# Performance work log

Measured on AMD Instinct MI355X. Metric: run time of the kernel, lower is better.

## Reference

```python
import jax, jax.numpy as jnp
import numpy as np

HEAD = 4
HW_DIM = 256  # in_dim // 2


def _gconv1x1(x, w, b):
    # groups=2 pointwise conv: x [B,C,H,W], w [O, C//2], b [O]
    B, C, H, W = x.shape
    O = w.shape[0]
    xg = x.reshape(B, 2, C // 2, H, W)
    wg = w.reshape(2, O // 2, C // 2)
    y = jnp.einsum('bgchw,goc->bgohw', xg, wg).reshape(B, O, H, W)
    return y + b[None, :, None, None]


def _bn_train(x, w, b, eps=1e-5):
    # BatchNorm2d in training mode (batch statistics over N,H,W)
    mean = x.mean(axis=(0, 2, 3), keepdims=True)
    var = ((x - mean) ** 2).mean(axis=(0, 2, 3), keepdims=True)
    return (x - mean) / jnp.sqrt(var + eps) * w[None, :, None, None] + b[None, :, None, None]


def _forward(x, wq, bq, wk, bk, wv, bv, bnh_w, bnh_b, bnw_w, bnw_b, gamma):
    B, C, H, W = x.shape
    org_x = x
    # first half of channels is detached in the original forward
    xd = jnp.concatenate([jax.lax.stop_gradient(x[:, :HW_DIM]), x[:, HW_DIM:]], axis=1)

    dqk_h = 512 // HEAD  # 128 per-head qk dim == `long`
    dv_h = 256 // HEAD   # 64 per-head value dim
    q = _gconv1x1(xd, wq, bq).reshape(B, HEAD, dqk_h, H, W)
    k = _gconv1x1(xd, wk, bk).reshape(B, HEAD, dqk_h, H, W)
    v = _gconv1x1(xd, wv, bv).reshape(B, HEAD, dv_h, H, W)
    scale = dqk_h ** (-0.5)

    # --- attention along H (per width column) ---
    eH = jnp.einsum('bnciw,bncjw->bnwij', q, k) * scale  # [B,HEAD,W,H,H]
    aH = jax.nn.softmax(eH, axis=-1)
    out_H = jnp.einsum('bnwij,bncjw->bnciw', aH, v).reshape(B, HEAD * dv_h, H, W)

    # --- attention along W (per height row) ---
    eW = jnp.einsum('bnchi,bnchj->bnhij', q, k) * scale  # [B,HEAD,H,W,W]
    aW = jax.nn.softmax(eW, axis=-1)
    out_W = jnp.einsum('bnhij,bnchj->bnchi', aW, v).reshape(B, HEAD * dv_h, H, W)

    p0 = _bn_train(out_H, bnh_w, bnh_b)[:, :HW_DIM // 2]
    p1 = _bn_train(out_W, bnw_w, bnw_b)[:, :HW_DIM // 2]

    out_temp = jnp.concatenate([out_H, out_W], axis=1)  # pre-BN outputs
    out = gamma * jax.nn.relu(out_temp) + org_x
    return out, p0, p1


def setup_inputs() -> dict:
    key = jax.random.key(0)
    ks = jax.random.split(key, 4)
    B, C, H, W = 4, 512, 128, 128
    s = 0.02
    return {
        'x': jax.random.normal(ks[0], (B, C, H, W), jnp.float32),
        'wq': jax.random.normal(ks[1], (512, 256), jnp.float32) * s,
        'bq': jnp.zeros((512,), jnp.float32),
        'wk': jax.random.normal(ks[2], (512, 256), jnp.float32) * s,
        'bk': jnp.zeros((512,), jnp.float32),
        'wv': jax.random.normal(ks[3], (256, 256), jnp.float32) * s,
        'bv': jnp.zeros((256,), jnp.float32),
        'bnh_w': jnp.ones((256,), jnp.float32),
        'bnh_b': jnp.zeros((256,), jnp.float32),
        'bnw_w': jnp.ones((256,), jnp.float32),
        'bnw_b': jnp.zeros((256,), jnp.float32),
        'gamma': jnp.full((1,), 0.1, jnp.float32),
    }


def reference(x, wq, bq, wk, bk, wv, bv, bnh_w, bnh_b, bnw_w, bnw_b, gamma):
    return _forward(x, wq, bq, wk, bk, wv, bv, bnh_w, bnh_b, bnw_w, bnw_b, gamma)
```

## Files before the change

kernel.cpp:

```cpp
#include <hip/hip_runtime.h>
#include <cstdint>
#include <cstddef>

constexpr int Bn = 4, Cin = 512, Hn = 128, Wn = 128, HWn = Hn * Wn;
constexpr float SCALE = 0.08838834764831845f;

typedef unsigned short u16;
typedef unsigned int u32;
using f32x4  = __attribute__((ext_vector_type(4))) float;
using bf16x8 = __attribute__((ext_vector_type(8))) short;

#define MFMA(a, b, c) __builtin_amdgcn_mfma_f32_16x16x32_bf16((a), (b), (c), 0, 0, 0)

__device__ __forceinline__ u16 bfu(float f) {
  u32 u = __float_as_uint(f);
  u += 0x7fffu + ((u >> 16) & 1u);
  return (u16)(u >> 16);
}

constexpr size_t SZ_XT = (size_t)Bn * HWn * 512 * 2;
constexpr size_t SZ_QK = (size_t)Bn * 4 * HWn * 128 * 2;
constexpr size_t SZ_V  = (size_t)Bn * 4 * HWn * 64 * 2;
constexpr size_t SZ_O  = (size_t)Bn * 256 * HWn * 4;
constexpr size_t OFF_XT = 0;
constexpr size_t OFF_Q  = OFF_XT + SZ_XT;
constexpr size_t OFF_K  = OFF_Q + SZ_QK;
constexpr size_t OFF_V  = OFF_K + SZ_QK;
constexpr size_t OFF_OH = OFF_V + SZ_V;
constexpr size_t OFF_OW = OFF_OH + SZ_O;
constexpr size_t OFF_ST = OFF_OW + SZ_O;

__global__ __launch_bounds__(256) void k_transpose_cast(const float* __restrict__ x,
                                                        u16* __restrict__ xT) {
  __shared__ float tile[32][33];
  const int b = blockIdx.z, c0 = blockIdx.y * 32, p0 = blockIdx.x * 32;
  const int t = threadIdx.x;
  const int pi = t & 31, ci = t >> 5;
  const float* xp = x + ((size_t)b * Cin + c0) * HWn + p0;
  for (int cc = ci; cc < 32; cc += 8) tile[cc][pi] = xp[(size_t)cc * HWn + pi];
  __syncthreads();
  u16* o = xT + ((size_t)b * HWn + p0) * Cin + c0;
  for (int pp = ci; pp < 32; pp += 8) o[(size_t)pp * Cin + pi] = bfu(tile[pi][pp]);
}

__global__ __launch_bounds__(256) void k_proj(
    const u16* __restrict__ xT,
    const float* __restrict__ wq, const float* __restrict__ bq,
    const float* __restrict__ wk, const float* __restrict__ bk,
    const float* __restrict__ wv, const float* __restrict__ bv,
    u16* __restrict__ Q, u16* __restrict__ K, u16* __restrict__ V) {
  __shared__ u16 sm[128 * 128 + 64 * 128];
  u16* xs = sm;
  u16* wsm = sm + 128 * 128;

  const int t = threadIdx.x;
  const int ot = blockIdx.x;
  const int pos0 = blockIdx.y * 128;
  const int b = blockIdx.z;

  const float* wsrc; const float* bsrc; u16* dst; int g, d0, pitch;
  if (ot < 8) {
    int qc0 = ot * 64; g = qc0 >> 8; int n = qc0 >> 7; d0 = qc0 & 127;
    wsrc = wq + (size_t)qc0 * 256; bsrc = bq + qc0;
    dst = Q + (size_t)(b * 4 + n) * HWn * 128; pitch = 128;
  } else if (ot < 16) {
    int kc0 = (ot - 8) * 64; g = kc0 >> 8; int n = kc0 >> 7; d0 = kc0 & 127;
    wsrc = wk + (size_t)kc0 * 256; bsrc = bk + kc0;
    dst = K + (size_t)(b * 4 + n) * HWn * 128; pitch = 128;
  } else {
    int vc0 = (ot - 16) * 64; g = vc0 >> 7; int n = vc0 >> 6; d0 = 0;
    wsrc = wv + (size_t)vc0 * 256; bsrc = bv + vc0;
    dst = V + (size_t)(b * 4 + n) * HWn * 64; pitch = 64;
  }

  const int lane = t & 63, wid = t >> 6, ln = lane & 15, qd = lane >> 4;
  const u16* xrow = xT + ((size_t)b * HWn + pos0) * 512 + g * 256;

  f32x4 acc[8];
#pragma unroll
  for (int i = 0; i < 8; ++i) acc[i] = f32x4{0.f, 0.f, 0.f, 0.f};

  for (int kc = 0; kc < 2; ++kc) {
    __syncthreads();
#pragma unroll
    for (int p = 0; p < 4; ++p) {
      int id = p * 256 + t;
      int oc = id >> 4, kb = id & 15;
      const float* wp = wsrc + (size_t)oc * 256 + kc * 128 + kb * 8;
      u32 pk0 = (u32)bfu(wp[0]) | ((u32)bfu(wp[1]) << 16);
      u32 pk1 = (u32)bfu(wp[2]) | ((u32)bfu(wp[3]) << 16);
      u32 pk2 = (u32)bfu(wp[4]) | ((u32)bfu(wp[5]) << 16);
      u32 pk3 = (u32)bfu(wp[6]) | ((u32)bfu(wp[7]) << 16);
      *(uint4*)&wsm[oc * 128 + (kb ^ (oc & 15)) * 8] = make_uint4(pk0, pk1, pk2, pk3);
    }
#pragma unroll
    for (int p = 0; p < 8; ++p) {
      int id = p * 256 + t;
      int pos = id >> 4, kb = id & 15;
      uint4 v = *(const uint4*)(xrow + (size_t)pos * 512 + kc * 128 + kb * 8);
      *(uint4*)&xs[pos * 128 + (kb ^ (pos & 15)) * 8] = v;
    }
    __syncthreads();
    const u16* arow = wsm + (wid * 16 + ln) * 128;
#pragma unroll
    for (int kk = 0; kk < 4; ++kk) {
      int kb = kk * 4 + qd;
      bf16x8 af = *(const bf16x8*)(arow + (kb ^ ln) * 8);
#pragma unroll
      for (int nt = 0; nt < 8; ++nt) {
        int prow = nt * 16 + ln;
        bf16x8 bf_ = *(const bf16x8*)(xs + prow * 128 + (kb ^ ln) * 8);
        acc[nt] = MFMA(af, bf_, acc[nt]);
      }
    }
  }
  __syncthreads();
  {
    float bias[4];
#pragma unroll
    for (int r = 0; r < 4; ++r) bias[r] = bsrc[wid * 16 + qd * 4 + r];
    int ocb = wid * 4 + qd;
#pragma unroll
    for (int nt = 0; nt < 8; ++nt) {
      int pos = nt * 16 + ln;
      u32 lo = (u32)bfu(acc[nt][0] + bias[0]) | ((u32)bfu(acc[nt][1] + bias[1]) << 16);
      u32 hi = (u32)bfu(acc[nt][2] + bias[2]) | ((u32)bfu(acc[nt][3] + bias[3]) << 16);
      *(uint2*)&wsm[pos * 64 + (ocb ^ (pos & 15)) * 4] = make_uint2(lo, hi);
    }
  }
  __syncthreads();
#pragma unroll
  for (int p = 0; p < 4; ++p) {
    int id = p * 256 + t;
    int pos = id >> 3, off = (id & 7) * 8;
    int ocb0 = off >> 2;
    uint2 g0 = *(const uint2*)&wsm[pos * 64 + ((ocb0) ^ (pos & 15)) * 4];
    uint2 g1 = *(const uint2*)&wsm[pos * 64 + ((ocb0 + 1) ^ (pos & 15)) * 4];
    *(uint4*)(dst + (size_t)(pos0 + pos) * pitch + d0 + off) = make_uint4(g0.x, g0.y, g1.x, g1.y);
  }
}

__global__ __launch_bounds__(256) void k_attn(
    const u16* __restrict__ Qg, const u16* __restrict__ Kg, const u16* __restrict__ Vg,
    float* __restrict__ outH, float* __restrict__ outW) {
  __shared__ u16 sm[64 * 128 + 128 * 128];
  u16* VT = sm;
  u16* KP = sm + 64 * 128;
  float* Os = (float*)KP;

  const int t = threadIdx.x;
  const int s = blockIdx.x;
  const int b = blockIdx.y >> 2, n = blockIdx.y & 3;
  const int dir = blockIdx.z;
  const int pos_base = (dir == 0) ? s : s * 128;
  const int step = (dir == 0) ? 128 : 1;

  const u16* qb = Qg + (size_t)(b * 4 + n) * HWn * 128;
  const u16* kb = Kg + (size_t)(b * 4 + n) * HWn * 128;
  const u16* vb = Vg + (size_t)(b * 4 + n) * HWn * 64;

#pragma unroll
  for (int p = 0; p < 8; ++p) {
    int id = p * 256 + t;
    int row = id >> 4, kk = id & 15;
    uint4 v = *(const uint4*)(kb + (size_t)(pos_base + row * step) * 128 + kk * 8);
    *(uint4*)&KP[row * 128 + (kk ^ (row & 15)) * 8] = v;
  }
#pragma unroll
  for (int p = 0; p < 4; ++p) {
    int id = p * 256 + t;
    int j = id >> 3, cb = id & 7;
    uint4 v = *(const uint4*)(vb + (size_t)(pos_base + j * step) * 64 + cb * 8);
    const u16* pv = (const u16*)&v;
    int jb = j >> 3, jr = j & 7;
#pragma unroll
    for (int e = 0; e < 8; ++e) {
      int c = cb * 8 + e;
      VT[c * 128 + (((jb ^ (c & 15)) << 3) | jr)] = pv[e];
    }
  }
  __syncthreads();

  const int lane = t & 63, wid = t >> 6, ln = lane & 15, qd = lane >> 4;
  f32x4 accS[2][8];
#pragma unroll
  for (int mi = 0; mi < 2; ++mi)
#pragma unroll
    for (int nt = 0; nt < 8; ++nt) accS[mi][nt] = f32x4{0.f, 0.f, 0.f, 0.f};

#pragma unroll
  for (int kk = 0; kk < 4; ++kk) {
    int kbi = kk * 4 + qd;
    bf16x8 a0 = *(const bf16x8*)(qb + (size_t)(pos_base + (wid * 32 + ln) * step) * 128 + kbi * 8);
    bf16x8 a1 = *(const bf16x8*)(qb + (size_t)(pos_base + (wid * 32 + 16 + ln) * step) * 128 + kbi * 8);
#pragma unroll
    for (int nt = 0; nt < 8; ++nt) {
      int row = nt * 16 + ln;
      bf16x8 bf_ = *(const bf16x8*)(KP + row * 128 + (kbi ^ ln) * 8);
      accS[0][nt] = MFMA(a0, bf_, accS[0][nt]);
      accS[1][nt] = MFMA(a1, bf_, accS[1][nt]);
    }
  }
  float rinv[2][4];
#pragma unroll
  for (int mi = 0; mi < 2; ++mi)
#pragma unroll
    for (int r = 0; r < 4; ++r) {
      float mx = accS[mi][0][r];
#pragma unroll
      for (int nt = 1; nt < 8; ++nt) mx = fmaxf(mx, accS[mi][nt][r]);
      mx = fmaxf(mx, __shfl_xor(mx, 1));
      mx = fmaxf(mx, __shfl_xor(mx, 2));
      mx = fmaxf(mx, __shfl_xor(mx, 4));
      mx = fmaxf(mx, __shfl_xor(mx, 8));
      float sum = 0.f;
#pragma unroll
      for (int nt = 0; nt < 8; ++nt) {
        float e = __expf((accS[mi][nt][r] - mx) * SCALE);
        accS[mi][nt][r] = e; sum += e;
      }
      sum += __shfl_xor(sum, 1);
      sum += __shfl_xor(sum, 2);
      sum += __shfl_xor(sum, 4);
      sum += __shfl_xor(sum, 8);
      rinv[mi][r] = 1.f / sum;
    }
  __syncthreads();
#pragma unroll
  for (int mi = 0; mi < 2; ++mi) {
    int mbase = (wid * 2 + mi) * 16 + qd * 4;
#pragma unroll
    for (int nt = 0; nt < 8; ++nt) {
      int nb = nt * 2 + (ln >> 3), nr = ln & 7;
#pragma unroll
      for (int r = 0; r < 4; ++r) {
        int m = mbase + r;
        KP[m * 128 + (((nb ^ (m & 15)) << 3) | nr)] = bfu(accS[mi][nt][r]);
      }
    }
  }
  f32x4 accO[2][4];
#pragma unroll
  for (int mi = 0; mi < 2; ++mi)
#pragma unroll
    for (int nt = 0; nt < 4; ++nt) accO[mi][nt] = f32x4{0.f, 0.f, 0.f, 0.f};
#pragma unroll
  for (int jj = 0; jj < 4; ++jj) {
    int jb2 = jj * 4 + qd;
    bf16x8 a0 = *(const bf16x8*)(KP + (wid * 32 + ln) * 128 + (jb2 ^ ln) * 8);
    bf16x8 a1 = *(const bf16x8*)(KP + (wid * 32 + 16 + ln) * 128 + (jb2 ^ ln) * 8);
#pragma unroll
    for (int nt = 0; nt < 4; ++nt) {
      int c = nt * 16 + ln;
      bf16x8 bf_ = *(const bf16x8*)(VT + c * 128 + (jb2 ^ (c & 15)) * 8);
      accO[0][nt] = MFMA(a0, bf_, accO[0][nt]);
      accO[1][nt] = MFMA(a1, bf_, accO[1][nt]);
    }
  }
  __syncthreads();
#pragma unroll
  for (int mi = 0; mi < 2; ++mi) {
    int ib = ((wid * 2 + mi) * 16 + qd * 4) >> 2;
#pragma unroll
    for (int nt = 0; nt < 4; ++nt) {
      int c = nt * 16 + ln;
      f32x4 v;
#pragma unroll
      for (int r = 0; r < 4; ++r) v[r] = accO[mi][nt][r] * rinv[mi][r];
      *(f32x4*)(Os + c * 128 + ((ib ^ (c & 31)) << 2)) = v;
    }
  }
  __syncthreads();
  float* obase; size_t cstride;
  if (dir == 0) { obase = outH + ((size_t)(b * 4 + n) * 128 + s) * 8192; cstride = 128; }
  else          { obase = outW + (size_t)(b * 256 + n * 64) * HWn + (size_t)s * 128; cstride = HWn; }
#pragma unroll
  for (int p = 0; p < 8; ++p) {
    int id = p * 256 + t;
    int c = id >> 5, i4 = id & 31;
    f32x4 v = *(const f32x4*)(Os + c * 128 + ((i4 ^ (c & 31)) << 2));
    *(f32x4*)(obase + (size_t)c * cstride + i4 * 4) = v;
  }
}

__global__ __launch_bounds__(256) void k_bnstats(const float* __restrict__ outH,
                                                 const float* __restrict__ outW,
                                                 float* __restrict__ stats) {
  const int cid = blockIdx.x;
  const int tensor = cid >> 7, ch = cid & 127;
  const int t = threadIdx.x;
  float s1 = 0.f, s2 = 0.f;
  if (tensor == 0) {
    const int n = ch >> 6, c = ch & 63;
    const int i = t & 127;
    for (int o = (t >> 7); o < 512; o += 2) {
      const int b = o >> 7, w = o & 127;
      float v = outH[(size_t)((b * 4 + n) * 128 + w) * 8192 + c * 128 + i];
      s1 += v; s2 += v * v;
    }
  } else {
    for (int f = t; f < 4 * HWn; f += 256) {
      const int b = f >> 14, p2 = f & (HWn - 1);
      float v = outW[(size_t)(b * 256 + ch) * HWn + p2];
      s1 += v; s2 += v * v;
    }
  }
#pragma unroll
  for (int m = 32; m >= 1; m >>= 1) { s1 += __shfl_xor(s1, m); s2 += __shfl_xor(s2, m); }
  __shared__ float r1[4], r2[4];
  if ((t & 63) == 0) { r1[t >> 6] = s1; r2[t >> 6] = s2; }
  __syncthreads();
  if (t == 0) {
    float a1 = r1[0] + r1[1] + r1[2] + r1[3];
    float a2 = r2[0] + r2[1] + r2[2] + r2[3];
    float mean = a1 * (1.f / 65536.f);
    float var = a2 * (1.f / 65536.f) - mean * mean;
    stats[tensor * 256 + ch] = mean;
    stats[tensor * 256 + 128 + ch] = rsqrtf(var + 1e-5f);
  }
}

__global__ __launch_bounds__(256) void k_final(
    const float* __restrict__ x, const float* __restrict__ outH,
    const float* __restrict__ outW, const float* __restrict__ stats,
    const float* __restrict__ bnh_w, const float* __restrict__ bnh_b,
    const float* __restrict__ bnw_w, const float* __restrict__ bnw_b,
    const float* __restrict__ gamma,
    float* __restrict__ out, float* __restrict__ p0, float* __restrict__ p1) {
  __shared__ float lds[32 * 129];
  const int t = threadIdx.x;
  const int w0 = blockIdx.x * 32;
  const int ch = blockIdx.y;
  const int b = blockIdx.z;
  const float gm = gamma[0];
  const float* xp = x + (size_t)(b * 512 + ch) * HWn;
  float* op = out + (size_t)(b * 512 + ch) * HWn;
  if (ch < 256) {
    const int n = ch >> 6, c = ch & 63;
    const float* hb = outH + (size_t)(b * 4 + n) * 128 * 8192 + c * 128;
    for (int ps = 0; ps < 16; ++ps) {
      int wl = ps * 2 + (t >> 7);
      lds[wl * 129 + (t & 127)] = hb[(size_t)(w0 + wl) * 8192 + (t & 127)];
    }
    __syncthreads();
    const bool dop = ch < 128;
    const float mean = dop ? stats[ch] : 0.f;
    const float istd = dop ? stats[128 + ch] : 0.f;
    const float bw = dop ? bnh_w[ch] : 0.f;
    const float bb = dop ? bnh_b[ch] : 0.f;
    float* pp = p0 + (size_t)(b * 128 + ch) * HWn;
    const int w = t & 31, h0 = t >> 5;
    for (int hh = 0; hh < 16; ++hh) {
      int h = hh * 8 + h0;
      float v = lds[w * 129 + h];
      int gi = h * 128 + w0 + w;
      op[gi] = gm * fmaxf(v, 0.f) + xp[gi];
      if (dop) pp[gi] = (v - mean) * istd * bw + bb;
    }
  } else {
    const int cw = ch - 256;
    const float* wbp = outW + (size_t)(b * 256 + cw) * HWn;
    const bool dop = cw < 128;
    const float mean = dop ? stats[256 + cw] : 0.f;
    const float istd = dop ? stats[384 + cw] : 0.f;
    const float bw = dop ? bnw_w[cw] : 0.f;
    const float bb = dop ? bnw_b[cw] : 0.f;
    float* pp = p1 + (size_t)(b * 128 + cw) * HWn;
    for (int it = 0; it < 16; ++it) {
      int fl = it * 256 + t;
      int h = fl >> 5, w = fl & 31;
      int gi = h * 128 + w0 + w;
      float v = wbp[gi];
      op[gi] = gm * fmaxf(v, 0.f) + xp[gi];
      if (dop) pp[gi] = (v - mean) * istd * bw + bb;
    }
  }
}

extern "C" void kernel_launch(void* const* d_in, const int* in_sizes, int n_in,
                              void* d_out, int out_size, void* d_ws, size_t ws_size,
                              hipStream_t stream) {
  (void)in_sizes; (void)n_in; (void)out_size; (void)ws_size;
  const float* x    = (const float*)d_in[0];
  const float* wq   = (const float*)d_in[1];
  const float* bq   = (const float*)d_in[2];
  const float* wk   = (const float*)d_in[3];
  const float* bk   = (const float*)d_in[4];
  const float* wv   = (const float*)d_in[5];
  const float* bv   = (const float*)d_in[6];
  const float* bnhw = (const float*)d_in[7];
  const float* bnhb = (const float*)d_in[8];
  const float* bnww = (const float*)d_in[9];
  const float* bnwb = (const float*)d_in[10];
  const float* gamma = (const float*)d_in[11];

  char* ws = (char*)d_ws;
  u16* xT = (u16*)(ws + OFF_XT);
  u16* Q  = (u16*)(ws + OFF_Q);
  u16* K  = (u16*)(ws + OFF_K);
  u16* V  = (u16*)(ws + OFF_V);
  float* oH = (float*)(ws + OFF_OH);
  float* oW = (float*)(ws + OFF_OW);
  float* st = (float*)(ws + OFF_ST);

  float* out = (float*)d_out;
  float* p0 = out + (size_t)Bn * 512 * HWn;
  float* p1 = p0 + (size_t)Bn * 128 * HWn;

  k_transpose_cast<<<dim3(512, 16, 4), 256, 0, stream>>>(x, xT);
  k_proj<<<dim3(20, 128, 4), 256, 0, stream>>>(xT, wq, bq, wk, bk, wv, bv, Q, K, V);
  k_attn<<<dim3(128, 16, 2), 256, 0, stream>>>(Q, K, V, oH, oW);
  k_bnstats<<<dim3(256), 256, 0, stream>>>(oH, oW, st);
  k_final<<<dim3(4, 512, 4), 256, 0, stream>>>(x, oH, oW, st, bnhw, bnhb, bnww, bnwb, gamma,
                                               out, p0, p1);
}
```

Measured before the change: 652.9 us.

## Precast weights once, widen projection tiles, fuse BN stats into attention

Weights and biases are now cast to bf16 once in an extra z-slice of the transpose kernel. The projection kernel then reads A fragments directly from global memory and computes 128 output channels per block instead of 64, which halves the block count and drops the repeated per-block weight conversion. The separate BN-statistics kernel is removed: the attention kernel accumulates per-channel sums and sums of squares with atomics, and the final kernel derives the mean and inverse std. Softmax now uses exp2 and a hardware reciprocal. The atomics and the E[x^2]-mean^2 variance formula add some numerical risk, and stats zeroing relies on the projection kernel running before attention.

```diff
diff --git a/kernel.cpp b/kernel.cpp
--- a/kernel.cpp
+++ b/kernel.cpp
@@ -3,7 +3,8 @@
 #include <cstddef>
 
 constexpr int Bn = 4, Cin = 512, Hn = 128, Wn = 128, HWn = Hn * Wn;
-constexpr float SCALE = 0.08838834764831845f;
+constexpr float SCALE_LOG2E = 0.12751743f;
+constexpr float INV_CNT = 1.52587890625e-05f;
 
 typedef unsigned short u16;
 typedef unsigned int u32;
@@ -29,12 +30,34 @@
 constexpr size_t OFF_OH = OFF_V + SZ_V;
 constexpr size_t OFF_OW = OFF_OH + SZ_O;
 constexpr size_t OFF_ST = OFF_OW + SZ_O;
-
-__global__ __launch_bounds__(256) void k_transpose_cast(const float* __restrict__ x,
-                                                        u16* __restrict__ xT) {
+constexpr size_t OFF_WB = OFF_ST + 4096;
+constexpr size_t OFF_BB = OFF_WB + (size_t)1280 * 256 * 2;
+
+__global__ __launch_bounds__(256) void k_transpose_cast(
+    const float* __restrict__ x,
+    const float* __restrict__ wq, const float* __restrict__ wk, const float* __restrict__ wv,
+    const float* __restrict__ bq, const float* __restrict__ bk, const float* __restrict__ bv,
+    u16* __restrict__ xT, u16* __restrict__ Wb, float* __restrict__ Bb) {
   __shared__ float tile[32][33];
+  const int t = threadIdx.x;
+  if (blockIdx.z == 4) {
+    if (blockIdx.y == 0 && blockIdx.x < 320) {
+      int idx = (blockIdx.x * 256 + t) * 4;
+      int row = idx >> 8, col = idx & 255;
+      const float* src = (row < 512)  ? (wq + (size_t)row * 256 + col)
+                       : (row < 1024) ? (wk + (size_t)(row - 512) * 256 + col)
+                                      : (wv + (size_t)(row - 1024) * 256 + col);
+      float4 v = *(const float4*)src;
+      u32 lo = (u32)bfu(v.x) | ((u32)bfu(v.y) << 16);
+      u32 hi = (u32)bfu(v.z) | ((u32)bfu(v.w) << 16);
+      *(uint2*)&Wb[idx] = make_uint2(lo, hi);
+    } else if (blockIdx.y == 1 && blockIdx.x == 0) {
+      for (int i = t; i < 1280; i += 256)
+        Bb[i] = (i < 512) ? bq[i] : (i < 1024) ? bk[i - 512] : bv[i - 1024];
+    }
+    return;
+  }
   const int b = blockIdx.z, c0 = blockIdx.y * 32, p0 = blockIdx.x * 32;
-  const int t = threadIdx.x;
   const int pi = t & 31, ci = t >> 5;
   const float* xp = x + ((size_t)b * Cin + c0) * HWn + p0;
   for (int cc = ci; cc < 32; cc += 8) tile[cc][pi] = xp[(size_t)cc * HWn + pi];
@@ -43,56 +66,33 @@
   for (int pp = ci; pp < 32; pp += 8) o[(size_t)pp * Cin + pi] = bfu(tile[pi][pp]);
 }
 
-__global__ __launch_bounds__(256) void k_proj(
-    const u16* __restrict__ xT,
-    const float* __restrict__ wq, const float* __restrict__ bq,
-    const float* __restrict__ wk, const float* __restrict__ bk,
-    const float* __restrict__ wv, const float* __restrict__ bv,
-    u16* __restrict__ Q, u16* __restrict__ K, u16* __restrict__ V) {
-  __shared__ u16 sm[128 * 128 + 64 * 128];
-  u16* xs = sm;
-  u16* wsm = sm + 128 * 128;
+__global__ __launch_bounds__(256, 3) void k_proj(
+    const u16* __restrict__ xT, const u16* __restrict__ Wb, const float* __restrict__ Bb,
+    u16* __restrict__ Q, u16* __restrict__ K, u16* __restrict__ V,
+    float* __restrict__ stats) {
+  __shared__ u16 xs[128 * 128];
 
   const int t = threadIdx.x;
   const int ot = blockIdx.x;
   const int pos0 = blockIdx.y * 128;
   const int b = blockIdx.z;
 
-  const float* wsrc; const float* bsrc; u16* dst; int g, d0, pitch;
-  if (ot < 8) {
-    int qc0 = ot * 64; g = qc0 >> 8; int n = qc0 >> 7; d0 = qc0 & 127;
-    wsrc = wq + (size_t)qc0 * 256; bsrc = bq + qc0;
-    dst = Q + (size_t)(b * 4 + n) * HWn * 128; pitch = 128;
-  } else if (ot < 16) {
-    int kc0 = (ot - 8) * 64; g = kc0 >> 8; int n = kc0 >> 7; d0 = kc0 & 127;
-    wsrc = wk + (size_t)kc0 * 256; bsrc = bk + kc0;
-    dst = K + (size_t)(b * 4 + n) * HWn * 128; pitch = 128;
-  } else {
-    int vc0 = (ot - 16) * 64; g = vc0 >> 7; int n = vc0 >> 6; d0 = 0;
-    wsrc = wv + (size_t)vc0 * 256; bsrc = bv + vc0;
-    dst = V + (size_t)(b * 4 + n) * HWn * 64; pitch = 64;
-  }
+  if (ot == 0 && blockIdx.y == 0 && b == 0) { stats[t] = 0.f; stats[256 + t] = 0.f; }
+
+  const int g = (ot < 8) ? ((ot & 3) >> 1) : (ot - 8);
+  const u16* xrow = xT + ((size_t)b * HWn + pos0) * 512 + g * 256;
 
   const int lane = t & 63, wid = t >> 6, ln = lane & 15, qd = lane >> 4;
-  const u16* xrow = xT + ((size_t)b * HWn + pos0) * 512 + g * 256;
-
-  f32x4 acc[8];
-#pragma unroll
-  for (int i = 0; i < 8; ++i) acc[i] = f32x4{0.f, 0.f, 0.f, 0.f};
+  const u16* wr0 = Wb + ((size_t)ot * 128 + wid * 32 + ln) * 256;
+
+  f32x4 acc[2][8];
+#pragma unroll
+  for (int mi = 0; mi < 2; ++mi)
+#pragma unroll
+    for (int nt = 0; nt < 8; ++nt) acc[mi][nt] = f32x4{0.f, 0.f, 0.f, 0.f};
 
   for (int kc = 0; kc < 2; ++kc) {
     __syncthreads();
-#pragma unroll
-    for (int p = 0; p < 4; ++p) {
-      int id = p * 256 + t;
-      int oc = id >> 4, kb = id & 15;
-      const float* wp = wsrc + (size_t)oc * 256 + kc * 128 + kb * 8;
-      u32 pk0 = (u32)bfu(wp[0]) | ((u32)bfu(wp[1]) << 16);
-      u32 pk1 = (u32)bfu(wp[2]) | ((u32)bfu(wp[3]) << 16);
-      u32 pk2 = (u32)bfu(wp[4]) | ((u32)bfu(wp[5]) << 16);
-      u32 pk3 = (u32)bfu(wp[6]) | ((u32)bfu(wp[7]) << 16);
-      *(uint4*)&wsm[oc * 128 + (kb ^ (oc & 15)) * 8] = make_uint4(pk0, pk1, pk2, pk3);
-    }
 #pragma unroll
     for (int p = 0; p < 8; ++p) {
       int id = p * 256 + t;
@@ -101,52 +101,76 @@
       *(uint4*)&xs[pos * 128 + (kb ^ (pos & 15)) * 8] = v;
     }
     __syncthreads();
-    const u16* arow = wsm + (wid * 16 + ln) * 128;
+    bf16x8 a[2][4];
 #pragma unroll
     for (int kk = 0; kk < 4; ++kk) {
-      int kb = kk * 4 + qd;
-      bf16x8 af = *(const bf16x8*)(arow + (kb ^ ln) * 8);
+      int kbi = kk * 4 + qd;
+      a[0][kk] = *(const bf16x8*)(wr0 + kc * 128 + kbi * 8);
+      a[1][kk] = *(const bf16x8*)(wr0 + 16 * 256 + kc * 128 + kbi * 8);
+    }
+#pragma unroll
+    for (int kk = 0; kk < 4; ++kk) {
+      int kbi = kk * 4 + qd;
 #pragma unroll
       for (int nt = 0; nt < 8; ++nt) {
-        int prow = nt * 16 + ln;
-        bf16x8 bf_ = *(const bf16x8*)(xs + prow * 128 + (kb ^ ln) * 8);
-        acc[nt] = MFMA(af, bf_, acc[nt]);
+        bf16x8 bf_ = *(const bf16x8*)(xs + (nt * 16 + ln) * 128 + (kbi ^ ln) * 8);
+        acc[0][nt] = MFMA(a[0][kk], bf_, acc[0][nt]);
+        acc[1][nt] = MFMA(a[1][kk], bf_, acc[1][nt]);
       }
     }
   }
   __syncthreads();
-  {
-    float bias[4];
-#pragma unroll
-    for (int r = 0; r < 4; ++r) bias[r] = bsrc[wid * 16 + qd * 4 + r];
-    int ocb = wid * 4 + qd;
+#pragma unroll
+  for (int mi = 0; mi < 2; ++mi) {
+    int oc = wid * 32 + mi * 16 + qd * 4;
+    const float* bp = Bb + ot * 128 + oc;
+    float b0 = bp[0], b1 = bp[1], b2 = bp[2], b3 = bp[3];
+    int ocb = oc >> 2;
 #pragma unroll
     for (int nt = 0; nt < 8; ++nt) {
       int pos = nt * 16 + ln;
-      u32 lo = (u32)bfu(acc[nt][0] + bias[0]) | ((u32)bfu(acc[nt][1] + bias[1]) << 16);
-      u32 hi = (u32)bfu(acc[nt][2] + bias[2]) | ((u32)bfu(acc[nt][3] + bias[3]) << 16);
-      *(uint2*)&wsm[pos * 64 + (ocb ^ (pos & 15)) * 4] = make_uint2(lo, hi);
-    }
-  }
-  __syncthreads();
-#pragma unroll
-  for (int p = 0; p < 4; ++p) {
-    int id = p * 256 + t;
-    int pos = id >> 3, off = (id & 7) * 8;
-    int ocb0 = off >> 2;
-    uint2 g0 = *(const uint2*)&wsm[pos * 64 + ((ocb0) ^ (pos & 15)) * 4];
-    uint2 g1 = *(const uint2*)&wsm[pos * 64 + ((ocb0 + 1) ^ (pos & 15)) * 4];
-    *(uint4*)(dst + (size_t)(pos0 + pos) * pitch + d0 + off) = make_uint4(g0.x, g0.y, g1.x, g1.y);
+      u32 lo = (u32)bfu(acc[mi][nt][0] + b0) | ((u32)bfu(acc[mi][nt][1] + b1) << 16);
+      u32 hi = (u32)bfu(acc[mi][nt][2] + b2) | ((u32)bfu(acc[mi][nt][3] + b3) << 16);
+      *(uint2*)&xs[pos * 128 + ((ocb ^ (pos & 31)) << 2)] = make_uint2(lo, hi);
+    }
+  }
+  __syncthreads();
+  if (ot < 8) {
+    u16* dst = (ot < 4) ? Q + (size_t)(b * 4 + ot) * HWn * 128
+                        : K + (size_t)(b * 4 + (ot - 4)) * HWn * 128;
+#pragma unroll
+    for (int p = 0; p < 8; ++p) {
+      int id = p * 256 + t;
+      int pos = id >> 4, grp = id & 15;
+      int s0 = (grp * 2) ^ (pos & 31), s1 = (grp * 2 + 1) ^ (pos & 31);
+      uint2 g0 = *(const uint2*)&xs[pos * 128 + (s0 << 2)];
+      uint2 g1 = *(const uint2*)&xs[pos * 128 + (s1 << 2)];
+      *(uint4*)(dst + (size_t)(pos0 + pos) * 128 + grp * 8) = make_uint4(g0.x, g0.y, g1.x, g1.y);
+    }
+  } else {
+    u16* vb = V + (size_t)(b * 4 + (ot - 8) * 2) * HWn * 64;
+#pragma unroll
+    for (int p = 0; p < 8; ++p) {
+      int id = p * 256 + t;
+      int pos = id >> 4, grp = id & 15;
+      int off = grp * 8;
+      int s0 = (grp * 2) ^ (pos & 31), s1 = (grp * 2 + 1) ^ (pos & 31);
+      uint2 g0 = *(const uint2*)&xs[pos * 128 + (s0 << 2)];
+      uint2 g1 = *(const uint2*)&xs[pos * 128 + (s1 << 2)];
+      u16* d = vb + (size_t)((off >> 6) * HWn + pos0 + pos) * 64 + (off & 63);
+      *(uint4*)d = make_uint4(g0.x, g0.y, g1.x, g1.y);
+    }
   }
 }
 
 __global__ __launch_bounds__(256) void k_attn(
     const u16* __restrict__ Qg, const u16* __restrict__ Kg, const u16* __restrict__ Vg,
-    float* __restrict__ outH, float* __restrict__ outW) {
+    float* __restrict__ outH, float* __restrict__ outW, float* __restrict__ stats) {
   __shared__ u16 sm[64 * 128 + 128 * 128];
   u16* VT = sm;
   u16* KP = sm + 64 * 128;
   float* Os = (float*)KP;
+  float* scr = (float*)VT;
 
   const int t = threadIdx.x;
   const int s = blockIdx.x;
@@ -216,14 +240,14 @@
       float sum = 0.f;
 #pragma unroll
       for (int nt = 0; nt < 8; ++nt) {
-        float e = __expf((accS[mi][nt][r] - mx) * SCALE);
+        float e = exp2f((accS[mi][nt][r] - mx) * SCALE_LOG2E);
         accS[mi][nt][r] = e; sum += e;
       }
       sum += __shfl_xor(sum, 1);
       sum += __shfl_xor(sum, 2);
       sum += __shfl_xor(sum, 4);
       sum += __shfl_xor(sum, 8);
-      rinv[mi][r] = 1.f / sum;
+      rinv[mi][r] = __builtin_amdgcn_rcpf(sum);
     }
   __syncthreads();
 #pragma unroll
@@ -258,6 +282,7 @@
     }
   }
   __syncthreads();
+  float s1[4] = {0.f, 0.f, 0.f, 0.f}, s2[4] = {0.f, 0.f, 0.f, 0.f};
 #pragma unroll
   for (int mi = 0; mi < 2; ++mi) {
     int ib = ((wid * 2 + mi) * 16 + qd * 4) >> 2;
@@ -267,10 +292,31 @@
       f32x4 v;
 #pragma unroll
       for (int r = 0; r < 4; ++r) v[r] = accO[mi][nt][r] * rinv[mi][r];
+      if (n < 2) {
+#pragma unroll
+        for (int r = 0; r < 4; ++r) { s1[nt] += v[r]; s2[nt] += v[r] * v[r]; }
+      }
       *(f32x4*)(Os + c * 128 + ((ib ^ (c & 31)) << 2)) = v;
     }
   }
-  __syncthreads();
+  if (n < 2) {
+#pragma unroll
+    for (int nt = 0; nt < 4; ++nt) {
+      float a = s1[nt]; a += __shfl_xor(a, 16); a += __shfl_xor(a, 32);
+      float q2 = s2[nt]; q2 += __shfl_xor(q2, 16); q2 += __shfl_xor(q2, 32);
+      if (qd == 0) {
+        scr[(wid * 2 + 0) * 64 + nt * 16 + ln] = a;
+        scr[(wid * 2 + 1) * 64 + nt * 16 + ln] = q2;
+      }
+    }
+  }
+  __syncthreads();
+  if (n < 2 && t < 128) {
+    int part = t >> 6, c2 = t & 63;
+    float v = scr[(0 * 2 + part) * 64 + c2] + scr[(1 * 2 + part) * 64 + c2] +
+              scr[(2 * 2 + part) * 64 + c2] + scr[(3 * 2 + part) * 64 + c2];
+    atomicAdd(&stats[dir * 256 + part * 128 + n * 64 + c2], v);
+  }
   float* obase; size_t cstride;
   if (dir == 0) { obase = outH + ((size_t)(b * 4 + n) * 128 + s) * 8192; cstride = 128; }
   else          { obase = outW + (size_t)(b * 256 + n * 64) * HWn + (size_t)s * 128; cstride = HWn; }
@@ -280,43 +326,6 @@
     int c = id >> 5, i4 = id & 31;
     f32x4 v = *(const f32x4*)(Os + c * 128 + ((i4 ^ (c & 31)) << 2));
     *(f32x4*)(obase + (size_t)c * cstride + i4 * 4) = v;
-  }
-}
-
-__global__ __launch_bounds__(256) void k_bnstats(const float* __restrict__ outH,
-                                                 const float* __restrict__ outW,
-                                                 float* __restrict__ stats) {
-  const int cid = blockIdx.x;
-  const int tensor = cid >> 7, ch = cid & 127;
-  const int t = threadIdx.x;
-  float s1 = 0.f, s2 = 0.f;
-  if (tensor == 0) {
-    const int n = ch >> 6, c = ch & 63;
-    const int i = t & 127;
-    for (int o = (t >> 7); o < 512; o += 2) {
-      const int b = o >> 7, w = o & 127;
-      float v = outH[(size_t)((b * 4 + n) * 128 + w) * 8192 + c * 128 + i];
-      s1 += v; s2 += v * v;
-    }
-  } else {
-    for (int f = t; f < 4 * HWn; f += 256) {
-      const int b = f >> 14, p2 = f & (HWn - 1);
-      float v = outW[(size_t)(b * 256 + ch) * HWn + p2];
-      s1 += v; s2 += v * v;
-    }
-  }
-#pragma unroll
-  for (int m = 32; m >= 1; m >>= 1) { s1 += __shfl_xor(s1, m); s2 += __shfl_xor(s2, m); }
-  __shared__ float r1[4], r2[4];
-  if ((t & 63) == 0) { r1[t >> 6] = s1; r2[t >> 6] = s2; }
-  __syncthreads();
-  if (t == 0) {
-    float a1 = r1[0] + r1[1] + r1[2] + r1[3];
-    float a2 = r2[0] + r2[1] + r2[2] + r2[3];
-    float mean = a1 * (1.f / 65536.f);
-    float var = a2 * (1.f / 65536.f) - mean * mean;
-    stats[tensor * 256 + ch] = mean;
-    stats[tensor * 256 + 128 + ch] = rsqrtf(var + 1e-5f);
   }
 }
 
@@ -344,10 +353,13 @@
     }
     __syncthreads();
     const bool dop = ch < 128;
-    const float mean = dop ? stats[ch] : 0.f;
-    const float istd = dop ? stats[128 + ch] : 0.f;
-    const float bw = dop ? bnh_w[ch] : 0.f;
-    const float bb = dop ? bnh_b[ch] : 0.f;
+    float mean = 0.f, istd = 0.f, bw = 0.f, bb = 0.f;
+    if (dop) {
+      mean = stats[ch] * INV_CNT;
+      float ex2 = stats[128 + ch] * INV_CNT;
+      istd = rsqrtf(fmaxf(ex2 - mean * mean, 0.f) + 1e-5f);
+      bw = bnh_w[ch]; bb = bnh_b[ch];
+    }
     float* pp = p0 + (size_t)(b * 128 + ch) * HWn;
     const int w = t & 31, h0 = t >> 5;
     for (int hh = 0; hh < 16; ++hh) {
@@ -361,10 +373,13 @@
     const int cw = ch - 256;
     const float* wbp = outW + (size_t)(b * 256 + cw) * HWn;
     const bool dop = cw < 128;
-    const float mean = dop ? stats[256 + cw] : 0.f;
-    const float istd = dop ? stats[384 + cw] : 0.f;
-    const float bw = dop ? bnw_w[cw] : 0.f;
-    const float bb = dop ? bnw_b[cw] : 0.f;
+    float mean = 0.f, istd = 0.f, bw = 0.f, bb = 0.f;
+    if (dop) {
+      mean = stats[256 + cw] * INV_CNT;
+      float ex2 = stats[384 + cw] * INV_CNT;
+      istd = rsqrtf(fmaxf(ex2 - mean * mean, 0.f) + 1e-5f);
+      bw = bnw_w[cw]; bb = bnw_b[cw];
+    }
     float* pp = p1 + (size_t)(b * 128 + cw) * HWn;
     for (int it = 0; it < 16; ++it) {
       int fl = it * 256 + t;
@@ -402,15 +417,16 @@
   float* oH = (float*)(ws + OFF_OH);
   float* oW = (float*)(ws + OFF_OW);
   float* st = (float*)(ws + OFF_ST);
+  u16* Wb = (u16*)(ws + OFF_WB);
+  float* Bb = (float*)(ws + OFF_BB);
 
   float* out = (float*)d_out;
   float* p0 = out + (size_t)Bn * 512 * HWn;
   float* p1 = p0 + (size_t)Bn * 128 * HWn;
 
-  k_transpose_cast<<<dim3(512, 16, 4), 256, 0, stream>>>(x, xT);
-  k_proj<<<dim3(20, 128, 4), 256, 0, stream>>>(xT, wq, bq, wk, bk, wv, bv, Q, K, V);
-  k_attn<<<dim3(128, 16, 2), 256, 0, stream>>>(Q, K, V, oH, oW);
-  k_bnstats<<<dim3(256), 256, 0, stream>>>(oH, oW, st);
+  k_transpose_cast<<<dim3(512, 16, 5), 256, 0, stream>>>(x, wq, wk, wv, bq, bk, bv, xT, Wb, Bb);
+  k_proj<<<dim3(10, 128, 4), 256, 0, stream>>>(xT, Wb, Bb, Q, K, V, st);
+  k_attn<<<dim3(128, 16, 2), 256, 0, stream>>>(Q, K, V, oH, oW, st);
   k_final<<<dim3(4, 512, 4), 256, 0, stream>>>(x, oH, oW, st, bnhw, bnhb, bnww, bnwb, gamma,
                                                out, p0, p1);
 }
```

Measured after the change: 577.5 us. -11.6%, faster.
